# Kernel optimization log

Hardware: AMD Instinct MI355X
Metric: run time of the kernel (lower is better)

## Reference

```python
import jax, jax.numpy as jnp
import numpy as np

NUM_HEADS = 16
EMBED = 1024
BLOCK = 2048
VOCAB = 32000
HEAD = EMBED // NUM_HEADS


def setup_inputs() -> dict:
    key = jax.random.key(0)
    ks = jax.random.split(key, 9)
    B, T = 2, 2048
    x = jax.random.randint(ks[0], (B, T), 0, VOCAB)
    target = jax.random.randint(ks[1], (B, T), 0, VOCAB)
    s = 0.02
    tok_emb = jax.random.normal(ks[2], (VOCAB, EMBED), jnp.float32) * s
    pos_emb = jax.random.normal(ks[3], (BLOCK, EMBED), jnp.float32) * s
    Wq = jax.random.normal(ks[4], (EMBED, EMBED), jnp.float32) * s
    Wk = jax.random.normal(ks[5], (EMBED, EMBED), jnp.float32) * s
    Wv = jax.random.normal(ks[6], (EMBED, EMBED), jnp.float32) * s
    W_lm = jax.random.normal(ks[7], (EMBED, VOCAB), jnp.float32) * s
    b_lm = jnp.zeros((VOCAB,), jnp.float32)
    return {"x": x, "target": target, "tok_emb": tok_emb, "pos_emb": pos_emb,
            "Wq": Wq, "Wk": Wk, "Wv": Wv, "W_lm": W_lm, "b_lm": b_lm}


def reference(x, target, tok_emb, pos_emb, Wq, Wk, Wv, W_lm, b_lm):
    B, T = x.shape
    h = tok_emb[x] + pos_emb[:T]                       # [B,T,E]
    # fused QKV projections, then split into heads (equivalent to per-head Linears + concat)
    q = (h @ Wq).reshape(B, T, NUM_HEADS, HEAD)
    k = (h @ Wk).reshape(B, T, NUM_HEADS, HEAD)
    v = (h @ Wv).reshape(B, T, NUM_HEADS, HEAD)
    scores = jnp.einsum("bqhd,bkhd->bhqk", q, k) / (HEAD ** 0.5)
    causal = jnp.tril(jnp.ones((T, T), bool))
    scores = jnp.where(causal, scores, -jnp.inf)
    attn = jax.nn.softmax(scores, axis=-1)             # [B,H,T,T]
    out = jnp.einsum("bhqk,bkhd->bqhd", attn, v).reshape(B, T, EMBED)
    logits = out @ W_lm + b_lm                         # [B,T,V]
    logits_flat = logits.reshape(B * T, VOCAB)
    logp = jax.nn.log_softmax(logits_flat, axis=-1)
    loss = -jnp.take_along_axis(logp, target.reshape(-1, 1), axis=-1).mean()
    return logits_flat, loss
```

## Files before the change

kernel.cpp:

```cpp
#include <hip/hip_runtime.h>
#include <cstdint>
#include <cstddef>

#define EMB   1024
#define TSEQ  2048
#define NBATCH 2
#define NHEAD 16
#define HDIM  64
#define VOCAB 32000
#define ROWS  4096
#define NCB   125

typedef __attribute__((ext_vector_type(8))) short short8;
typedef __attribute__((ext_vector_type(4))) float f32x4;

__device__ __forceinline__ unsigned short f2bf(float f) {
  unsigned int u = __float_as_uint(f);
  u = (u + 0x7FFFu + ((u >> 16) & 1u)) >> 16;
  return (unsigned short)u;
}

__device__ __forceinline__ void gload16(const void* g, void* l) {
  typedef __attribute__((address_space(1))) const unsigned int gu;
  typedef __attribute__((address_space(3))) unsigned int lu;
  __builtin_amdgcn_global_load_lds((gu*)g, (lu*)l, 16, 0, 0);
}

__global__ void convT(const float* __restrict__ in, unsigned short* __restrict__ out,
                      int R, int C) {
  __shared__ float tile[32][33];
  const int ct = blockIdx.x, rt = blockIdx.y;
  const int t = threadIdx.x;
  const int r0 = t >> 5;
  const int c  = t & 31;
#pragma unroll
  for (int i = 0; i < 4; ++i) {
    int r = r0 + i * 8;
    tile[r][c] = in[(size_t)(rt * 32 + r) * C + ct * 32 + c];
  }
  __syncthreads();
#pragma unroll
  for (int i = 0; i < 4; ++i) {
    int r = r0 + i * 8;
    out[(size_t)(ct * 32 + r) * R + rt * 32 + c] = f2bf(tile[c][r]);
  }
}

__global__ void embed_kernel(const int* __restrict__ x, const float* __restrict__ tok,
                             const float* __restrict__ pos, unsigned short* __restrict__ h) {
  const int idx = blockIdx.x * 256 + threadIdx.x;
  const int row = idx >> 8;
  const int c4  = idx & 255;
  const int tpos = row & (TSEQ - 1);
  const int token = x[row];
  float4 a = *(const float4*)(tok + (size_t)token * EMB + c4 * 4);
  float4 p = *(const float4*)(pos + (size_t)tpos * EMB + c4 * 4);
  unsigned int lo = (unsigned int)f2bf(a.x + p.x) | ((unsigned int)f2bf(a.y + p.y) << 16);
  unsigned int hi = (unsigned int)f2bf(a.z + p.z) | ((unsigned int)f2bf(a.w + p.w) << 16);
  *(uint2*)(h + (size_t)idx * 4) = make_uint2(lo, hi);
}

template <int EPI>
__global__ void gemm_bt(const unsigned short* __restrict__ A,
                        const unsigned short* __restrict__ Bt,
                        void* __restrict__ Cout,
                        float scale, int M, int N, int K) {
  __shared__ unsigned short As[2][128 * 32];
  __shared__ unsigned short Bs[2][128 * 32];
  const int t  = threadIdx.x;
  const int l  = t & 63;
  const int w  = t >> 6;
  const int wr = w >> 1, wc = w & 1;
  const int m0 = blockIdx.y * 128;
  const int n0 = blockIdx.x * 128;
  const int KT = K >> 5;

  f32x4 acc[4][4] = {};

  const int crow = t >> 2;
  const int coff = (t & 3) * 16;
  const size_t abase = ((size_t)(m0 + crow) * K) * 2 + coff;
  const size_t bbase = ((size_t)(n0 + crow) * K) * 2 + coff;
  const size_t rstep = (size_t)64 * K * 2;
  const char* Ab = (const char*)A;
  const char* Bb = (const char*)Bt;

#define STAGE(buf, kt_) do {                                              \
    size_t ko = (size_t)(kt_) * 64;                                       \
    gload16(Ab + abase + ko,         (char*)&As[(buf)][0] + t * 16);      \
    gload16(Ab + abase + rstep + ko, (char*)&As[(buf)][0] + t * 16 + 4096);\
    gload16(Bb + bbase + ko,         (char*)&Bs[(buf)][0] + t * 16);      \
    gload16(Bb + bbase + rstep + ko, (char*)&Bs[(buf)][0] + t * 16 + 4096);\
  } while (0)

  const int lr  = l & 15;
  const int lkb = (l >> 4) * 16;

#define COMPUTE(buf) do {                                                  \
    const char* ab = (const char*)&As[(buf)][0];                           \
    const char* bb = (const char*)&Bs[(buf)][0];                           \
    short8 fa[4], fb[4];                                                   \
    _Pragma("unroll")                                                      \
    for (int m = 0; m < 4; ++m)                                            \
      fa[m] = *(const short8*)(ab + (wr * 64 + m * 16 + lr) * 64 + lkb);   \
    _Pragma("unroll")                                                      \
    for (int n = 0; n < 4; ++n)                                            \
      fb[n] = *(const short8*)(bb + (wc * 64 + n * 16 + lr) * 64 + lkb);   \
    _Pragma("unroll")                                                      \
    for (int m = 0; m < 4; ++m)                                            \
      _Pragma("unroll")                                                    \
      for (int n = 0; n < 4; ++n)                                          \
        acc[m][n] = __builtin_amdgcn_mfma_f32_16x16x32_bf16(               \
            fa[m], fb[n], acc[m][n], 0, 0, 0);                             \
  } while (0)

  STAGE(0, 0);
  __syncthreads();
  int cur = 0;
  for (int kt = 0; kt < KT; ++kt) {
    if (kt + 1 < KT) STAGE(cur ^ 1, kt + 1);
    COMPUTE(cur);
    __syncthreads();
    cur ^= 1;
  }
#undef STAGE
#undef COMPUTE

  const int orow = m0 + wr * 64 + (l >> 4) * 4;
  const int ocol = n0 + wc * 64 + lr;
#pragma unroll
  for (int m = 0; m < 4; ++m) {
#pragma unroll
    for (int n = 0; n < 4; ++n) {
      const int col = ocol + n * 16;
      if (EPI == 1) {
        unsigned short* C = (unsigned short*)Cout;
#pragma unroll
        for (int r = 0; r < 4; ++r) {
          int row = orow + m * 16 + r;
          C[(size_t)row * N + col] = f2bf(acc[m][n][r] * scale);
        }
      } else {
        unsigned short* C = (unsigned short*)Cout;
        int row0 = orow + m * 16;
        int bb_ = row0 >> 11, tq = row0 & 2047;
        int hh = col >> 6, dd = col & 63;
        unsigned int lo = (unsigned int)f2bf(acc[m][n][0]) | ((unsigned int)f2bf(acc[m][n][1]) << 16);
        unsigned int hi = (unsigned int)f2bf(acc[m][n][2]) | ((unsigned int)f2bf(acc[m][n][3]) << 16);
        *(uint2*)&C[(((size_t)(bb_ * NHEAD + hh) * HDIM + dd) * TSEQ) + tq] = make_uint2(lo, hi);
      }
    }
  }
}

__global__ __launch_bounds__(256)
void attn_mfma(const unsigned short* __restrict__ Qbf,
               const unsigned short* __restrict__ Kbf,
               const unsigned short* __restrict__ Vtbf,
               unsigned short* __restrict__ Obf) {
  const int qt = (gridDim.x - 1) - blockIdx.x;
  const int h  = blockIdx.y;
  const int b  = blockIdx.z;
  const int t  = threadIdx.x, w = t >> 6, l = t & 63;
  const int g  = l >> 4, c = l & 15;
  const int qw = qt * 64 + w * 16;
  const int qg = qw + c;

  __shared__ unsigned short Ks[2][32 * 64];
  __shared__ unsigned short Vs[2][64 * 32];

  const unsigned short* Qrow = Qbf + ((size_t)(b * TSEQ + qg) * EMB + h * HDIM);
  short8 qfrag[2];
  qfrag[0] = *(const short8*)(Qrow + g * 8);
  qfrag[1] = *(const short8*)(Qrow + g * 8 + 32);

  f32x4 accO[4] = {};
  float mrun = -3e38f, lsum = 0.0f;

  const int kvt = t >> 3, kch = t & 7;
  const char* Kg = (const char*)(Kbf + ((size_t)(b * TSEQ + kvt) * EMB + h * HDIM))
                   + (((kch * 16) ^ ((kvt & 7) << 4)));
  const int dt = t >> 2, vch = t & 3;
  const char* Vg = (const char*)(Vtbf + (((size_t)(b * NHEAD + h) * HDIM + dt) * TSEQ))
                   + vch * 16;
  const size_t kstep = (size_t)32 * EMB * 2;
  const size_t vstep = (size_t)32 * 2;

#define ASTAGE(buf, kt_) do {                                               \
    gload16(Kg + (size_t)(kt_) * kstep, (char*)&Ks[buf][0] + t * 16);       \
    gload16(Vg + (size_t)(kt_) * vstep, (char*)&Vs[buf][0] + t * 16);       \
  } while (0)

  const int nkt = 2 * qt + 2;
  ASTAGE(0, 0);
  __syncthreads();
  int cur = 0;
  for (int kt = 0; kt < nkt; ++kt) {
    if (kt + 1 < nkt) ASTAGE(cur ^ 1, kt + 1);
    const int k0 = kt * 32;

    const char* kb = (const char*)&Ks[cur][0];
    f32x4 sa[2] = {};
#pragma unroll
    for (int kc = 0; kc < 2; ++kc) {
#pragma unroll
      for (int kh = 0; kh < 2; ++kh) {
        short8 ka = *(const short8*)(kb + (kc * 16 + c) * 128 +
                                     ((g * 16 + kh * 64) ^ ((c & 7) << 4)));
        sa[kc] = __builtin_amdgcn_mfma_f32_16x16x32_bf16(ka, qfrag[kh], sa[kc], 0, 0, 0);
      }
    }

    float sv[8];
#pragma unroll
    for (int kc = 0; kc < 2; ++kc)
#pragma unroll
      for (int r = 0; r < 4; ++r) {
        int kv = k0 + kc * 16 + g * 4 + r;
        sv[kc * 4 + r] = (kv > qg) ? -3e38f : sa[kc][r];
      }
    float pm = sv[0];
#pragma unroll
    for (int i = 1; i < 8; ++i) pm = fmaxf(pm, sv[i]);
    pm = fmaxf(pm, __shfl_xor(pm, 16));
    pm = fmaxf(pm, __shfl_xor(pm, 32));
    const float mnew = fmaxf(mrun, pm);
    const float alpha = __expf(mrun - mnew);
    float ps = 0.0f;
#pragma unroll
    for (int i = 0; i < 8; ++i) { float p = __expf(sv[i] - mnew); sv[i] = p; ps += p; }
    ps += __shfl_xor(ps, 16);
    ps += __shfl_xor(ps, 32);
    lsum = lsum * alpha + ps;
    mrun = mnew;

#pragma unroll
    for (int r = 0; r < 4; ++r) {
      float ar = __shfl(alpha, g * 4 + r);
      accO[0][r] *= ar; accO[1][r] *= ar; accO[2][r] *= ar; accO[3][r] *= ar;
    }

    unsigned int wf[4];
#pragma unroll
    for (int rp = 0; rp < 2; ++rp)
#pragma unroll
      for (int kc = 0; kc < 2; ++kc) {
        unsigned int rw;
        asm("v_cvt_pk_bf16_f32 %0, %1, %2"
            : "=v"(rw) : "v"(sv[kc * 4 + 2 * rp]), "v"(sv[kc * 4 + 2 * rp + 1]));
        wf[rp * 2 + kc] = rw;
      }

    union { unsigned int u[4]; short8 s8; } pa;
#pragma unroll
    for (int jp = 0; jp < 4; ++jp) {
      int srcLane = c + ((2 * (g & 1) + (jp >> 1)) << 4);
      unsigned int v0 = (unsigned int)__shfl((int)wf[2 * (jp & 1)], srcLane);
      unsigned int v1 = (unsigned int)__shfl((int)wf[2 * (jp & 1) + 1], srcLane);
      pa.u[jp] = (g >> 1) ? v1 : v0;
    }

    const char* vb = (const char*)&Vs[cur][0];
#pragma unroll
    for (int cp = 0; cp < 4; ++cp) {
      short8 vf = *(const short8*)(vb + (c + 16 * cp) * 64 + g * 16);
      accO[cp] = __builtin_amdgcn_mfma_f32_16x16x32_bf16(pa.s8, vf, accO[cp], 0, 0, 0);
    }

    __syncthreads();
    cur ^= 1;
  }
#undef ASTAGE

  const float inv = 1.0f / lsum;
#pragma unroll
  for (int r = 0; r < 4; ++r) {
    float ir = __shfl(inv, g * 4 + r);
    unsigned short* orow = Obf + ((size_t)(b * TSEQ + qw + g * 4 + r) * EMB + h * HDIM);
#pragma unroll
    for (int cp = 0; cp < 4; ++cp)
      orow[c + 16 * cp] = f2bf(accO[cp][r] * ir);
  }
}

__global__ __launch_bounds__(1024)
void gemm_lm(const unsigned short* __restrict__ A,
             const unsigned short* __restrict__ Bt,
             const float* __restrict__ bias,
             float* __restrict__ C,
             float* __restrict__ pm, float* __restrict__ ps) {
  extern __shared__ char lds[];
  const int t = threadIdx.x;
  const int w = t >> 6, l = t & 63;
  const int wm = w >> 2, wn = w & 3;
  const int fr = l & 15, kg = l >> 4;

  const int L  = blockIdx.x;
  const int Lp = (L & 7) * 250 + (L >> 3);
  const int mtile = Lp & 15;
  const int ntile = Lp >> 4;

  const char* Ag = (const char*)A;
  const char* Bg = (const char*)Bt;

  const int srow = t >> 3;
  const int sch  = (t & 7) ^ (srow & 7);
  const unsigned int aoff0 = ((unsigned int)(mtile * 256 + srow) * EMB) * 2 + sch * 16;
  const unsigned int boff0 = ((unsigned int)(ntile * 256 + srow) * EMB) * 2 + sch * 16;
  const int sd = t * 16;

#define STG_A(buf_, kt_) do {                                               \
    char* d_ = lds + (buf_) * 65536 + sd;                                   \
    gload16(Ag + aoff0 + (kt_) * 128, d_);                                  \
    gload16(Ag + aoff0 + 262144u + (kt_) * 128, d_ + 16384);                \
  } while (0)
#define STG_B(buf_, kt_) do {                                               \
    char* d_ = lds + (buf_) * 65536 + 32768 + sd;                           \
    gload16(Bg + boff0 + (kt_) * 128, d_);                                  \
    gload16(Bg + boff0 + 262144u + (kt_) * 128, d_ + 16384);                \
  } while (0)

  const int xr  = fr & 7;
  const int cb0 = (kg ^ xr) * 16;
  const int arow = (wm * 64 + fr) * 128;
  const int brow = (wn * 64 + fr) * 128;

  f32x4 acc[4][4] = {};
  short8 fa[2][2], fb[4][2];

#define PH_MFMA(MH)                                                          \
  _Pragma("unroll")                                                          \
  for (int mi = 0; mi < 2; ++mi)                                             \
    _Pragma("unroll")                                                        \
    for (int ni = 0; ni < 4; ++ni)                                           \
      _Pragma("unroll")                                                      \
      for (int ks = 0; ks < 2; ++ks)                                         \
        acc[(MH)*2+mi][ni] = __builtin_amdgcn_mfma_f32_16x16x32_bf16(        \
            fa[mi][ks], fb[ni][ks], acc[(MH)*2+mi][ni], 0, 0, 0);

#define TILE(h_, SA, SB, VMN) do {                                           \
    const int p_ = (h_) & 1;                                                 \
    const char* Ab_ = lds + p_ * 65536;                                      \
    const char* Bb_ = Ab_ + 32768;                                           \
                                                          \
    _Pragma("unroll")                                                        \
    for (int mi = 0; mi < 2; ++mi) {                                         \
      fa[mi][0] = *(const short8*)(Ab_ + arow + mi * 2048 + cb0);            \
      fa[mi][1] = *(const short8*)(Ab_ + arow + mi * 2048 + (cb0 ^ 64));     \
    }                                                                        \
    _Pragma("unroll")                                                        \
    for (int ni = 0; ni < 4; ++ni) {                                         \
      fb[ni][0] = *(const short8*)(Bb_ + brow + ni * 2048 + cb0);            \
      fb[ni][1] = *(const short8*)(Bb_ + brow + ni * 2048 + (cb0 ^ 64));     \
    }                                                                        \
    if (SA) STG_A(p_ ^ 1, (h_) + 1);                                         \
    __builtin_amdgcn_s_barrier();                                            \
    __builtin_amdgcn_s_setprio(1); PH_MFMA(0); __builtin_amdgcn_s_setprio(0);\
    __builtin_amdgcn_s_barrier();                                            \
                                                          \
    _Pragma("unroll")                                                        \
    for (int mi = 0; mi < 2; ++mi) {                                         \
      fa[mi][0] = *(const short8*)(Ab_ + arow + (2 + mi) * 2048 + cb0);      \
      fa[mi][1] = *(const short8*)(Ab_ + arow + (2 + mi) * 2048 + (cb0 ^ 64));\
    }                                                                        \
    if (SB) STG_B(p_, (h_) + 2);                                             \
    __builtin_amdgcn_s_barrier();                                            \
    __builtin_amdgcn_s_setprio(1); PH_MFMA(1); __builtin_amdgcn_s_setprio(0);\
    asm volatile("s_waitcnt vmcnt(" #VMN ")" ::: "memory");                  \
    __builtin_amdgcn_s_barrier();                                            \
  } while (0)

  STG_A(0, 0); STG_B(0, 0); STG_B(1, 1);
  asm volatile("s_waitcnt vmcnt(2)" ::: "memory");
  __builtin_amdgcn_s_barrier();

  for (int h = 0; h < 14; ++h) TILE(h, 1, 1, 2);
  TILE(14, 1, 0, 0);
  TILE(15, 0, 0, 0);
#undef TILE
#undef PH_MFMA
#undef STG_A
#undef STG_B

  __syncthreads();

  const int mrow0 = mtile * 256 + wm * 64;
  const int ncol0 = ntile * 256 + wn * 64;
  float biasv[4];
#pragma unroll
  for (int ni = 0; ni < 4; ++ni) biasv[ni] = bias[ncol0 + ni * 16 + fr];
#pragma unroll
  for (int mi = 0; mi < 4; ++mi)
#pragma unroll
    for (int ni = 0; ni < 4; ++ni)
#pragma unroll
      for (int rr = 0; rr < 4; ++rr)
        acc[mi][ni][rr] += biasv[ni];

#pragma unroll
  for (int mi = 0; mi < 4; ++mi)
#pragma unroll
    for (int rr = 0; rr < 4; ++rr) {
      int row = mrow0 + mi * 16 + kg * 4 + rr;
      float* cr = C + (size_t)row * VOCAB + ncol0 + fr;
#pragma unroll
      for (int ni = 0; ni < 4; ++ni) cr[ni * 16] = acc[mi][ni][rr];
    }

  float* redm = (float*)lds;
  float* reds = (float*)(lds + 4096);
#pragma unroll
  for (int mi = 0; mi < 4; ++mi)
#pragma unroll
    for (int rr = 0; rr < 4; ++rr) {
      float m1 = fmaxf(fmaxf(acc[mi][0][rr], acc[mi][1][rr]),
                       fmaxf(acc[mi][2][rr], acc[mi][3][rr]));
      m1 = fmaxf(m1, __shfl_xor(m1, 1));
      m1 = fmaxf(m1, __shfl_xor(m1, 2));
      m1 = fmaxf(m1, __shfl_xor(m1, 4));
      m1 = fmaxf(m1, __shfl_xor(m1, 8));
      if (fr == 0) redm[wn * 256 + wm * 64 + mi * 16 + kg * 4 + rr] = m1;
    }
  __syncthreads();

  float rmx[4][4];
#pragma unroll
  for (int mi = 0; mi < 4; ++mi)
#pragma unroll
    for (int rr = 0; rr < 4; ++rr) {
      int row = wm * 64 + mi * 16 + kg * 4 + rr;
      float a0 = fmaxf(redm[0 * 256 + row], redm[1 * 256 + row]);
      float a1 = fmaxf(redm[2 * 256 + row], redm[3 * 256 + row]);
      rmx[mi][rr] = fmaxf(a0, a1);
    }
#pragma unroll
  for (int mi = 0; mi < 4; ++mi)
#pragma unroll
    for (int rr = 0; rr < 4; ++rr) {
      float r = rmx[mi][rr];
      float s1 = __expf(acc[mi][0][rr] - r) + __expf(acc[mi][1][rr] - r)
               + __expf(acc[mi][2][rr] - r) + __expf(acc[mi][3][rr] - r);
      s1 += __shfl_xor(s1, 1);
      s1 += __shfl_xor(s1, 2);
      s1 += __shfl_xor(s1, 4);
      s1 += __shfl_xor(s1, 8);
      if (fr == 0) reds[wn * 256 + wm * 64 + mi * 16 + kg * 4 + rr] = s1;
    }
  __syncthreads();

  if (wn == 0 && fr == 0) {
#pragma unroll
    for (int mi = 0; mi < 4; ++mi)
#pragma unroll
      for (int rr = 0; rr < 4; ++rr) {
        int row = wm * 64 + mi * 16 + kg * 4 + rr;
        float ssum = reds[0 * 256 + row] + reds[1 * 256 + row]
                   + reds[2 * 256 + row] + reds[3 * 256 + row];
        int grow = mtile * 256 + row;
        pm[(size_t)grow * NCB + ntile] = rmx[mi][rr];
        ps[(size_t)grow * NCB + ntile] = ssum;
      }
  }
}

__global__ void loss_rows2(const float* __restrict__ pm, const float* __restrict__ ps,
                           const float* __restrict__ logits, const int* __restrict__ tgt,
                           float* __restrict__ partial) {
  const int row = blockIdx.x * 4 + (threadIdx.x >> 6);
  const int l = threadIdx.x & 63;
  const float* pmr = pm + (size_t)row * NCB;
  const float* psr = ps + (size_t)row * NCB;
  float m = -3e38f, s = 0.0f;
  for (int i = l; i < NCB; i += 64) {
    float mv = pmr[i], sv = psr[i];
    float nm = fmaxf(m, mv);
    s = s * __expf(m - nm) + sv * __expf(mv - nm);
    m = nm;
  }
#pragma unroll
  for (int off = 1; off < 64; off <<= 1) {
    float om = __shfl_xor(m, off), os = __shfl_xor(s, off);
    float nm = fmaxf(m, om);
    s = s * __expf(m - nm) + os * __expf(om - nm);
    m = nm;
  }
  if (l == 0) {
    float lse = m + __logf(s);
    partial[row] = -(logits[(size_t)row * VOCAB + tgt[row]] - lse);
  }
}

__global__ void loss_final(const float* __restrict__ partial, float* __restrict__ out) {
  const int t = threadIdx.x;
  float s = 0.0f;
  for (int i = t; i < ROWS; i += 256) s += partial[i];
#pragma unroll
  for (int off = 1; off < 64; off <<= 1) s += __shfl_xor(s, off);
  __shared__ float ws_[4];
  if ((t & 63) == 0) ws_[t >> 6] = s;
  __syncthreads();
  if (t == 0) out[0] = (ws_[0] + ws_[1] + ws_[2] + ws_[3]) * (1.0f / (float)ROWS);
}

extern "C" void kernel_launch(void* const* d_in, const int* in_sizes, int n_in,
                              void* d_out, int out_size, void* d_ws, size_t ws_size,
                              hipStream_t stream) {
  const int*   x      = (const int*)d_in[0];
  const int*   target = (const int*)d_in[1];
  const float* tok    = (const float*)d_in[2];
  const float* pos    = (const float*)d_in[3];
  const float* Wq     = (const float*)d_in[4];
  const float* Wk     = (const float*)d_in[5];
  const float* Wv     = (const float*)d_in[6];
  const float* Wlm    = (const float*)d_in[7];
  const float* blm    = (const float*)d_in[8];
  float* out = (float*)d_out;

  char* p = (char*)d_ws;
  unsigned short* Wqt  = (unsigned short*)p; p += (size_t)EMB * EMB * 2;
  unsigned short* Wkt  = (unsigned short*)p; p += (size_t)EMB * EMB * 2;
  unsigned short* Wvt  = (unsigned short*)p; p += (size_t)EMB * EMB * 2;
  unsigned short* Wlmt = (unsigned short*)p; p += (size_t)VOCAB * EMB * 2;
  unsigned short* hbf  = (unsigned short*)p; p += (size_t)ROWS * EMB * 2;
  unsigned short* qbf  = (unsigned short*)p; p += (size_t)ROWS * EMB * 2;
  unsigned short* kbf  = (unsigned short*)p; p += (size_t)ROWS * EMB * 2;
  unsigned short* vtbf = (unsigned short*)p; p += (size_t)ROWS * EMB * 2;
  unsigned short* obf  = (unsigned short*)p; p += (size_t)ROWS * EMB * 2;
  float*          prt  = (float*)p;          p += (size_t)ROWS * 4;
  float*          pmw  = (float*)p;          p += (size_t)ROWS * NCB * 4;
  float*          psw  = (float*)p;          p += (size_t)ROWS * NCB * 4;

  hipFuncSetAttribute((const void*)gemm_lm,
                      hipFuncAttributeMaxDynamicSharedMemorySize, 131072);

  dim3 b256(256);
  convT<<<dim3(EMB / 32, EMB / 32), b256, 0, stream>>>(Wq, Wqt, EMB, EMB);
  convT<<<dim3(EMB / 32, EMB / 32), b256, 0, stream>>>(Wk, Wkt, EMB, EMB);
  convT<<<dim3(EMB / 32, EMB / 32), b256, 0, stream>>>(Wv, Wvt, EMB, EMB);
  convT<<<dim3(VOCAB / 32, EMB / 32), b256, 0, stream>>>(Wlm, Wlmt, EMB, VOCAB);

  embed_kernel<<<ROWS * (EMB / 4) / 256, b256, 0, stream>>>(x, tok, pos, hbf);

  gemm_bt<1><<<dim3(EMB / 128, ROWS / 128), b256, 0, stream>>>(hbf, Wqt, qbf, 0.125f, ROWS, EMB, EMB);
  gemm_bt<1><<<dim3(EMB / 128, ROWS / 128), b256, 0, stream>>>(hbf, Wkt, kbf, 1.0f, ROWS, EMB, EMB);
  gemm_bt<2><<<dim3(EMB / 128, ROWS / 128), b256, 0, stream>>>(hbf, Wvt, vtbf, 1.0f, ROWS, EMB, EMB);

  attn_mfma<<<dim3(TSEQ / 64, NHEAD, NBATCH), b256, 0, stream>>>(qbf, kbf, vtbf, obf);

  gemm_lm<<<dim3((ROWS / 256) * (VOCAB / 256)), dim3(1024), 131072, stream>>>(
      obf, Wlmt, blm, out, pmw, psw);

  loss_rows2<<<ROWS / 4, b256, 0, stream>>>(pmw, psw, out, target, prt);
  loss_final<<<1, b256, 0, stream>>>(prt, out + (size_t)ROWS * VOCAB);
}
```

Baseline: 711.3 us.

## Stage LM-head logits through LDS for coalesced nontemporal stores and remap tile order

The LM-head GEMM epilogue now writes accumulators into a swizzled LDS buffer in two 128-row halves, then has each thread emit contiguous 16-byte nontemporal stores of the fp32 logits. This replaces scattered 4-byte per-lane stores. The block-to-tile mapping also changes so that groups of 4 M-tiles share each N-tile within a stripe, which targets better L2 reuse of the weight tiles. The cost is extra LDS traffic and barriers in the epilogue.

```diff
diff --git a/kernel.cpp b/kernel.cpp
--- a/kernel.cpp
+++ b/kernel.cpp
@@ -295,10 +295,12 @@
   const int wm = w >> 2, wn = w & 3;
   const int fr = l & 15, kg = l >> 4;
 
-  const int L  = blockIdx.x;
-  const int Lp = (L & 7) * 250 + (L >> 3);
-  const int mtile = Lp & 15;
-  const int ntile = Lp >> 4;
+  const int L   = blockIdx.x;
+  const int Lp  = (L & 7) * 250 + (L >> 3);
+  const int stripe = Lp / 500;
+  const int rr_ = Lp % 500;
+  const int ntile = rr_ >> 2;
+  const int mtile = stripe * 4 + (rr_ & 3);
 
   const char* Ag = (const char*)A;
   const char* Bg = (const char*)Bt;
@@ -397,16 +399,6 @@
       for (int rr = 0; rr < 4; ++rr)
         acc[mi][ni][rr] += biasv[ni];
 
-#pragma unroll
-  for (int mi = 0; mi < 4; ++mi)
-#pragma unroll
-    for (int rr = 0; rr < 4; ++rr) {
-      int row = mrow0 + mi * 16 + kg * 4 + rr;
-      float* cr = C + (size_t)row * VOCAB + ncol0 + fr;
-#pragma unroll
-      for (int ni = 0; ni < 4; ++ni) cr[ni * 16] = acc[mi][ni][rr];
-    }
-
   float* redm = (float*)lds;
   float* reds = (float*)(lds + 4096);
 #pragma unroll
@@ -460,6 +452,43 @@
         pm[(size_t)grow * NCB + ntile] = rmx[mi][rr];
         ps[(size_t)grow * NCB + ntile] = ssum;
       }
+  }
+  __syncthreads();
+
+  float* ld = (float*)lds;
+  const int erow = t >> 3;
+  const int ecg  = t & 7;
+#pragma unroll
+  for (int Hh = 0; Hh < 2; ++Hh) {
+    if ((wm >> 1) == Hh) {
+      const int rbase = (wm & 1) * 64;
+#pragma unroll
+      for (int mi = 0; mi < 4; ++mi)
+#pragma unroll
+        for (int rr = 0; rr < 4; ++rr) {
+          const int row = rbase + mi * 16 + kg * 4 + rr;
+#pragma unroll
+          for (int ni = 0; ni < 4; ++ni) {
+            const int col = wn * 64 + ni * 16 + fr;
+            const int phys = (((col >> 2) ^ (row & 7)) << 2) | (col & 3);
+            ld[row * 256 + phys] = acc[mi][ni][rr];
+          }
+        }
+    }
+    __syncthreads();
+    {
+      const int grow = mtile * 256 + Hh * 128 + erow;
+      float* gp = C + (size_t)grow * VOCAB + ntile * 256 + ecg * 32;
+      const float* lp = ld + erow * 256;
+#pragma unroll
+      for (int j = 0; j < 8; ++j) {
+        const int col4 = ecg * 8 + j;
+        const int phys4 = col4 ^ (erow & 7);
+        f32x4 v = *(const f32x4*)(lp + phys4 * 4);
+        __builtin_nontemporal_store(v, (f32x4*)(gp + j * 4));
+      }
+    }
+    __syncthreads();
   }
 }
 
```

After: 1.980 ms. 178% more time.
